# Kernel tuning notes

Hardware: AMD Instinct MI355X
Metric: run time of the kernel (lower is better)

## Reference

```python
import jax, jax.numpy as jnp
import numpy as np

N = 100000
E = 1600000
D_IN = 128
D_OUT = 128

def setup_inputs() -> dict:
    key = jax.random.key(0)
    k1, k2, k3, k4, k5, k6 = jax.random.split(key, 6)
    h = jax.random.normal(k1, (N, D_IN), dtype=jnp.float32)
    # norm ~ deg^{-1/2}; use positive uniform values as stand-in
    norm = jax.random.uniform(k2, (N, 1), dtype=jnp.float32, minval=0.05, maxval=1.0)
    src = jax.random.randint(k3, (E,), 0, N, dtype=jnp.int32)
    dst = jax.random.randint(k4, (E,), 0, N, dtype=jnp.int32)
    weight = jax.random.normal(k5, (D_IN, D_OUT), dtype=jnp.float32) * (2.0 / (D_IN + D_OUT)) ** 0.5
    bias = jnp.zeros((D_OUT,), dtype=jnp.float32)
    return {"h": h, "norm": norm, "src": src, "dst": dst, "weight": weight, "bias": bias}

def reference(h, norm, src, dst, weight, bias):
    n_nodes = h.shape[0]
    hw = h @ weight                      # [N, D_out] dense GEMM
    hw = hw * norm                       # pre-aggregation degree scale
    msgs = hw[src]                       # gather: [E, D_out]
    agg = jax.ops.segment_sum(msgs, dst, num_segments=n_nodes)  # scatter-sum
    out = agg * norm + bias              # post-scale + bias
    return out
```

## Files before the change

### kernel.cpp

```cpp
#include <hip/hip_runtime.h>
#include <hip/hip_bf16.h>

#define D 128
#define D4 32
#define CHUNK 3072
#define MAXB 2048
#define NSEG 8
#define SL 4096

typedef __attribute__((ext_vector_type(8))) short bf16x8;
typedef __attribute__((ext_vector_type(8))) unsigned short ushort8;
typedef __attribute__((ext_vector_type(4))) float f32x4;

static __device__ __forceinline__ unsigned short f2bf(float f) {
    unsigned u = __float_as_uint(f);
    u += 0x7FFFu + ((u >> 16) & 1u);
    return (unsigned short)(u >> 16);
}
static __device__ __forceinline__ float bf2f(unsigned short u) {
    return __uint_as_float(((unsigned)u) << 16);
}

__global__ __launch_bounds__(256) void wcvt_kernel(
    const float* __restrict__ W, unsigned short* __restrict__ Wt)
{
    const int idx = blockIdx.x * 256 + threadIdx.x;
    const float4 w = ((const float4*)W)[idx];
    const int k = idx >> 5;
    const int c = (idx & 31) * 4;
    Wt[(c + 0) * 128 + k] = f2bf(w.x);
    Wt[(c + 1) * 128 + k] = f2bf(w.y);
    Wt[(c + 2) * 128 + k] = f2bf(w.z);
    Wt[(c + 3) * 128 + k] = f2bf(w.w);
}

__global__ __launch_bounds__(512) void gemm_mfma_kernel(
    const float* __restrict__ h, const unsigned short* __restrict__ Wt,
    const float* __restrict__ norm, unsigned short* __restrict__ hwb,
    int n_nodes)
{
    __shared__ unsigned short Bs[128 * 136];

    const int t = threadIdx.x;
    const int row0 = blockIdx.x * 128;

    #pragma unroll
    for (int i = 0; i < 4; ++i) {
        const int idx = t + 512 * i;
        const int c = idx >> 4;
        const int k8 = idx & 15;
        *(ushort8*)&Bs[c * 136 + k8 * 8] = ((const ushort8*)Wt)[idx];
    }
    __syncthreads();

    const int wv = t >> 6;
    const int lane = t & 63;
    const int m = lane & 15;
    const int quad = lane >> 4;

    long gra = row0 + wv * 16 + m;
    if (gra >= n_nodes) gra = n_nodes - 1;
    const float* hrow = h + gra * D;

    f32x4 acc[8];
    #pragma unroll
    for (int nt = 0; nt < 8; ++nt) { f32x4 z = {0.f, 0.f, 0.f, 0.f}; acc[nt] = z; }

    #pragma unroll
    for (int kt = 0; kt < 4; ++kt) {
        const float4 a0 = *(const float4*)(hrow + kt * 32 + quad * 8);
        const float4 a1 = *(const float4*)(hrow + kt * 32 + quad * 8 + 4);
        bf16x8 af;
        unsigned short* ap = (unsigned short*)&af;
        ap[0] = f2bf(a0.x); ap[1] = f2bf(a0.y); ap[2] = f2bf(a0.z); ap[3] = f2bf(a0.w);
        ap[4] = f2bf(a1.x); ap[5] = f2bf(a1.y); ap[6] = f2bf(a1.z); ap[7] = f2bf(a1.w);
        #pragma unroll
        for (int nt = 0; nt < 8; ++nt) {
            const bf16x8 bfr = *(const bf16x8*)&Bs[(nt * 16 + m) * 136 + kt * 32 + quad * 8];
            acc[nt] = __builtin_amdgcn_mfma_f32_16x16x32_bf16(af, bfr, acc[nt], 0, 0, 0);
        }
    }

    float nv[4];
    #pragma unroll
    for (int i = 0; i < 4; ++i) {
        const int gr = row0 + wv * 16 + quad * 4 + i;
        nv[i] = (gr < n_nodes) ? norm[gr] : 0.f;
    }
    #pragma unroll
    for (int nt = 0; nt < 8; ++nt) {
        #pragma unroll
        for (int i = 0; i < 4; ++i) {
            const int gr = row0 + wv * 16 + quad * 4 + i;
            if (gr < n_nodes)
                hwb[(size_t)gr * D + nt * 16 + m] = f2bf(acc[nt][i] * nv[i]);
        }
    }
}

__global__ __launch_bounds__(1024) void hist_kernel(
    const int* __restrict__ dst, int* __restrict__ H,
    unsigned short* __restrict__ hwb, int n_edges, int n_nodes)
{
    __shared__ int lbh[MAXB];
    const int t = threadIdx.x;
    const int g = blockIdx.x;
    for (int i = t; i < MAXB; i += 1024) lbh[i] = 0;
    if (g == 0 && t < 32) {
        ushort4 z; z.x = z.y = z.z = z.w = 0;
        ((ushort4*)(hwb + (size_t)n_nodes * D))[t] = z;
    }
    __syncthreads();
    const int e0 = g * CHUNK;
    const int e1 = min(e0 + CHUNK, n_edges);
    for (int e = e0 + t; e < e1; e += 1024) {
        atomicAdd(&lbh[dst[e] >> 6], 1);
    }
    __syncthreads();
    for (int i = t; i < MAXB; i += 1024) {
        H[(size_t)g * MAXB + i] = lbh[i];
    }
}

__global__ __launch_bounds__(256) void colsum_kernel(
    const int* __restrict__ H, int* __restrict__ PS, int eb)
{
    const int col = blockIdx.x * 256 + threadIdx.x;
    const int seg = blockIdx.y;
    const int glen = (eb + NSEG - 1) / NSEG;
    const int g0 = seg * glen;
    const int g1 = min(g0 + glen, eb);
    int s = 0;
    for (int g = g0; g < g1; ++g) s += H[(size_t)g * MAXB + col];
    PS[seg * MAXB + col] = s;
}

__global__ __launch_bounds__(256) void bucket_scan_kernel(
    const int* __restrict__ PS, int* __restrict__ boff, int* __restrict__ SB)
{
    __shared__ int tmp[256];
    const int t = threadIdx.x;
    int v[8];
    int s = 0;
    #pragma unroll
    for (int k = 0; k < 8; ++k) {
        const int i = t * 8 + k;
        int c = 0;
        #pragma unroll
        for (int sg = 0; sg < NSEG; ++sg) c += PS[sg * MAXB + i];
        v[k] = c; s += c;
    }
    tmp[t] = s;
    __syncthreads();
    for (int ofs = 1; ofs < 256; ofs <<= 1) {
        int x = (t >= ofs) ? tmp[t - ofs] : 0;
        __syncthreads();
        tmp[t] += x;
        __syncthreads();
    }
    int run = tmp[t] - s;
    #pragma unroll
    for (int k = 0; k < 8; ++k) {
        const int i = t * 8 + k;
        boff[i] = run;
        int sb = run;
        #pragma unroll
        for (int sg = 0; sg < NSEG; ++sg) {
            SB[sg * MAXB + i] = sb;
            sb += PS[sg * MAXB + i];
        }
        run += v[k];
    }
    if (t == 255) boff[MAXB] = run;
}

__global__ __launch_bounds__(256) void chunkscan_kernel(
    const int* __restrict__ H, const int* __restrict__ SB,
    int* __restrict__ CO, int eb)
{
    const int b = blockIdx.x * 256 + threadIdx.x;
    const int seg = blockIdx.y;
    const int glen = (eb + NSEG - 1) / NSEG;
    const int g0 = seg * glen;
    const int g1 = min(g0 + glen, eb);
    int run = SB[seg * MAXB + b];
    for (int g = g0; g < g1; ++g) {
        CO[(size_t)g * MAXB + b] = run;
        run += H[(size_t)g * MAXB + b];
    }
}

__global__ __launch_bounds__(1024) void bscatter_kernel(
    const int* __restrict__ src, const int* __restrict__ dst,
    const int* __restrict__ CO,
    unsigned int* __restrict__ ebuf, int n_edges)
{
    __shared__ int lbh[MAXB];
    __shared__ int lofs[MAXB];
    const int t = threadIdx.x;
    const int g = blockIdx.x;
    for (int i = t; i < MAXB; i += 1024) {
        lbh[i] = 0;
        lofs[i] = CO[(size_t)g * MAXB + i];
    }
    __syncthreads();
    const int e0 = g * CHUNK;
    const int e1 = min(e0 + CHUNK, n_edges);
    for (int e = e0 + t; e < e1; e += 1024) {
        const int d = dst[e];
        const int bk = d >> 6;
        const int r = atomicAdd(&lbh[bk], 1);
        ebuf[lofs[bk] + r] = (unsigned)src[e] | ((unsigned)(d & 63) << 17);
    }
}

__global__ __launch_bounds__(256) void fillagg_kernel(
    const unsigned int* __restrict__ ebuf, const int* __restrict__ boff,
    int* __restrict__ srcs_g, const unsigned short* __restrict__ hwb,
    const float* __restrict__ norm, const float* __restrict__ bias,
    float* __restrict__ out, int n_nodes)
{
    __shared__ int slds[SL];
    __shared__ int lcnt[64];
    __shared__ int lcur[64];
    __shared__ int loff[64];
    const int t = threadIdx.x;
    const int b = blockIdx.x;
    const int gn0 = b * 64;

    if (t < 64) lcnt[t] = 0;
    __syncthreads();
    const int w0 = boff[b], w1 = boff[b + 1];
    const int wlen = w1 - w0;
    const bool uselds = (wlen + 480) <= SL;
    const int gbase = w0 + 448 * b;

    for (int e = w0 + t; e < w1; e += 256) {
        atomicAdd(&lcnt[(ebuf[e] >> 17) & 63], 1);
    }
    __syncthreads();
    if (t < 64) {
        const int c = lcnt[t];
        const int p = (c + 7) & ~7;
        int x = p;
        #pragma unroll
        for (int ofs = 1; ofs < 64; ofs <<= 1) {
            const int y = __shfl_up(x, ofs, 64);
            if (t >= ofs) x += y;
        }
        const int base = x - p;
        lcur[t] = base;
        loff[t] = base;
    }
    __syncthreads();
    for (int e = w0 + t; e < w1; e += 256) {
        const unsigned rec = ebuf[e];
        const int loc = (rec >> 17) & 63;
        const int pos = atomicAdd(&lcur[loc], 1);
        const int sv = (int)(rec & 0x1FFFFu);
        if (uselds) slds[pos] = sv; else srcs_g[gbase + pos] = sv;
    }
    for (int w = t; w < 512; w += 256) {
        const int ln = w >> 3, k = w & 7;
        const int gn = gn0 + ln;
        if (gn < n_nodes) {
            const int c = lcnt[ln];
            const int pad = (8 - (c & 7)) & 7;
            if (k < pad) {
                const int pos = loff[ln] + c + k;
                if (uselds) slds[pos] = n_nodes; else srcs_g[gbase + pos] = n_nodes;
            }
        }
    }
    __syncthreads();

    const ushort4* hw4 = (const ushort4*)hwb;
    const int grp = t >> 5;
    const int l = t & 31;
    const float4 bs = ((const float4*)bias)[l];
    for (int nn = 0; nn < 8; ++nn) {
        const int loc = grp * 8 + nn;
        const int gn = gn0 + loc;
        if (gn >= n_nodes) continue;
        const int start = loff[loc];
        const int deg = lcnt[loc];
        const int nb8 = (deg + 7) >> 3;
        float4 acc; acc.x = acc.y = acc.z = acc.w = 0.f;
        int myidx = 0;
        for (int bb = 0; bb < nb8; ++bb) {
            const int q = bb & 3;
            if (q == 0) {
                const int ri = start + bb * 8 + l;
                myidx = uselds ? slds[ri] : srcs_g[gbase + ri];
            }
            ushort4 v[8];
            #pragma unroll
            for (int jj = 0; jj < 8; ++jj) {
                const int s = __shfl(myidx, q * 8 + jj, 32);
                v[jj] = hw4[(long)s * D4 + l];
            }
            #pragma unroll
            for (int jj = 0; jj < 8; ++jj) {
                acc.x += bf2f(v[jj].x);
                acc.y += bf2f(v[jj].y);
                acc.z += bf2f(v[jj].z);
                acc.w += bf2f(v[jj].w);
            }
        }
        const float nv = norm[gn];
        float4 o;
        o.x = acc.x * nv + bs.x;
        o.y = acc.y * nv + bs.y;
        o.z = acc.z * nv + bs.z;
        o.w = acc.w * nv + bs.w;
        ((float4*)out)[(long)gn * D4 + l] = o;
    }
}

__global__ __launch_bounds__(256) void scatter_kernel(
    const unsigned short* __restrict__ hwb, const int* __restrict__ src,
    const int* __restrict__ dst, float* __restrict__ out, int n_edges)
{
    const int idx = blockIdx.x * 256 + threadIdx.x;
    if (idx >= n_edges * D4) return;
    const int e = idx >> 5;
    const int g = idx & 31;
    const int s = src[e];
    const int d = dst[e];
    const ushort4 v = ((const ushort4*)hwb)[(long)s * D4 + g];
    float* o = out + (long)d * D + g * 4;
    atomicAdd(o + 0, bf2f(v.x));
    atomicAdd(o + 1, bf2f(v.y));
    atomicAdd(o + 2, bf2f(v.z));
    atomicAdd(o + 3, bf2f(v.w));
}

__global__ __launch_bounds__(256) void finalize_kernel(
    float* __restrict__ out, const float* __restrict__ norm,
    const float* __restrict__ bias, int n_nodes)
{
    const int idx = blockIdx.x * 256 + threadIdx.x;
    if (idx >= n_nodes * D4) return;
    const int n = idx >> 5;
    const int g = idx & 31;
    float4 v = ((float4*)out)[idx];
    const float nv = norm[n];
    const float4 b = ((const float4*)bias)[g];
    v.x = v.x * nv + b.x;
    v.y = v.y * nv + b.y;
    v.z = v.z * nv + b.z;
    v.w = v.w * nv + b.w;
    ((float4*)out)[idx] = v;
}

extern "C" void kernel_launch(void* const* d_in, const int* in_sizes, int n_in,
                              void* d_out, int out_size, void* d_ws, size_t ws_size,
                              hipStream_t stream) {
    const float* h    = (const float*)d_in[0];
    const float* norm = (const float*)d_in[1];
    const int*   src  = (const int*)d_in[2];
    const int*   dst  = (const int*)d_in[3];
    const float* W    = (const float*)d_in[4];
    const float* bias = (const float*)d_in[5];
    float* out = (float*)d_out;

    const int n_nodes = in_sizes[1];
    const int n_edges = in_sizes[2];

    const int NBUCK = (n_nodes + 63) >> 6;
    const int EB    = (n_edges + CHUNK - 1) / CHUNK;
    const int srcs_len = n_edges + 448 * NBUCK + 64;

    size_t p = 0;
    auto take = [&](size_t bytes) {
        size_t cur = p;
        p += (bytes + 255) & ~(size_t)255;
        return cur;
    };
    const size_t hwb_off  = take(((size_t)n_nodes + 1) * D * sizeof(unsigned short));
    const size_t wt_off   = take((size_t)D * D * sizeof(unsigned short));
    const size_t srcs_off = take((size_t)srcs_len * sizeof(int));
    const size_t ebuf_off = take((size_t)n_edges * sizeof(unsigned int));
    const size_t boff_off = take((MAXB + 1) * sizeof(int));
    const size_t H_off    = take((size_t)EB * MAXB * sizeof(int));
    const size_t PS_off   = take((size_t)NSEG * MAXB * sizeof(int));
    const size_t SB_off   = take((size_t)NSEG * MAXB * sizeof(int));
    const size_t CO_off   = take((size_t)EB * MAXB * sizeof(int));
    const size_t needed = p;

    char* ws = (char*)d_ws;
    unsigned short* hwb = (unsigned short*)(ws + hwb_off);
    unsigned short* Wt  = (unsigned short*)(ws + wt_off);

    wcvt_kernel<<<16, 256, 0, stream>>>(W, Wt);
    gemm_mfma_kernel<<<(n_nodes + 127) / 128, 512, 0, stream>>>(h, Wt, norm, hwb, n_nodes);

    if (ws_size >= needed && NBUCK <= MAXB && n_nodes <= 131072 && EB <= 1024) {
        int* srcs  = (int*)(ws + srcs_off);
        unsigned int* ebuf = (unsigned int*)(ws + ebuf_off);
        int* boff  = (int*)(ws + boff_off);
        int* H     = (int*)(ws + H_off);
        int* PS    = (int*)(ws + PS_off);
        int* SBp   = (int*)(ws + SB_off);
        int* CO    = (int*)(ws + CO_off);

        hist_kernel<<<EB, 1024, 0, stream>>>(dst, H, hwb, n_edges, n_nodes);
        colsum_kernel<<<dim3(MAXB / 256, NSEG), 256, 0, stream>>>(H, PS, EB);
        bucket_scan_kernel<<<1, 256, 0, stream>>>(PS, boff, SBp);
        chunkscan_kernel<<<dim3(MAXB / 256, NSEG), 256, 0, stream>>>(H, SBp, CO, EB);
        bscatter_kernel<<<EB, 1024, 0, stream>>>(src, dst, CO, ebuf, n_edges);
        fillagg_kernel<<<NBUCK, 256, 0, stream>>>(ebuf, boff, srcs, hwb, norm, bias,
                                                  out, n_nodes);
    } else {
        hipMemsetAsync(d_out, 0, (size_t)out_size * sizeof(float), stream);
        const int work = n_edges * D4;
        scatter_kernel<<<(work + 255) / 256, 256, 0, stream>>>(hwb, src, dst, out, n_edges);
        const int work2 = n_nodes * D4;
        finalize_kernel<<<(work2 + 255) / 256, 256, 0, stream>>>(out, norm, bias, n_nodes);
    }
}
```

Measured before the change: 247.1 us.

## Fuse colsum into local chunk scan, stage GEMM output via LDS, double chunk size

Merges the column-sum and chunk-scan passes into one kernel that writes chunk-local offsets plus segment totals, and adds the segment base inside the scatter kernel. This removes one kernel launch and one full pass over the histogram matrix. The GEMM epilogue now stages the bf16 results in shared memory and writes 16-byte vectors per row instead of scattered 2-byte stores. The edge chunk per block is also doubled, which halves the histogram and offset matrix sizes but gives each block more serial work and fewer blocks.

```diff
diff --git a/kernel.cpp b/kernel.cpp
--- a/kernel.cpp
+++ b/kernel.cpp
@@ -3,7 +3,7 @@
 
 #define D 128
 #define D4 32
-#define CHUNK 3072
+#define CHUNK 6144
 #define MAXB 2048
 #define NSEG 8
 #define SL 4096
@@ -87,14 +87,27 @@
         const int gr = row0 + wv * 16 + quad * 4 + i;
         nv[i] = (gr < n_nodes) ? norm[gr] : 0.f;
     }
+
+    __syncthreads();
     #pragma unroll
     for (int nt = 0; nt < 8; ++nt) {
         #pragma unroll
         for (int i = 0; i < 4; ++i) {
-            const int gr = row0 + wv * 16 + quad * 4 + i;
-            if (gr < n_nodes)
-                hwb[(size_t)gr * D + nt * 16 + m] = f2bf(acc[nt][i] * nv[i]);
-        }
+            const int r = wv * 16 + quad * 4 + i;
+            Bs[r * 136 + nt * 16 + m] = f2bf(acc[nt][i] * nv[i]);
+        }
+    }
+    __syncthreads();
+
+    #pragma unroll
+    for (int i2 = 0; i2 < 4; ++i2) {
+        const int idx = t + 512 * i2;
+        const int r = idx >> 4;
+        const int c8 = idx & 15;
+        const int gr = row0 + r;
+        if (gr < n_nodes)
+            *(ushort8*)&hwb[(size_t)gr * D + c8 * 8] =
+                *(const ushort8*)&Bs[r * 136 + c8 * 8];
     }
 }
 
@@ -122,17 +135,21 @@
     }
 }
 
-__global__ __launch_bounds__(256) void colsum_kernel(
-    const int* __restrict__ H, int* __restrict__ PS, int eb)
-{
-    const int col = blockIdx.x * 256 + threadIdx.x;
+__global__ __launch_bounds__(256) void chunkscan_local_kernel(
+    const int* __restrict__ H, int* __restrict__ CO, int* __restrict__ PS,
+    int eb)
+{
+    const int b = blockIdx.x * 256 + threadIdx.x;
     const int seg = blockIdx.y;
     const int glen = (eb + NSEG - 1) / NSEG;
     const int g0 = seg * glen;
     const int g1 = min(g0 + glen, eb);
-    int s = 0;
-    for (int g = g0; g < g1; ++g) s += H[(size_t)g * MAXB + col];
-    PS[seg * MAXB + col] = s;
+    int run = 0;
+    for (int g = g0; g < g1; ++g) {
+        CO[(size_t)g * MAXB + b] = run;
+        run += H[(size_t)g * MAXB + b];
+    }
+    PS[seg * MAXB + b] = run;
 }
 
 __global__ __launch_bounds__(256) void bucket_scan_kernel(
@@ -174,34 +191,20 @@
     if (t == 255) boff[MAXB] = run;
 }
 
-__global__ __launch_bounds__(256) void chunkscan_kernel(
-    const int* __restrict__ H, const int* __restrict__ SB,
-    int* __restrict__ CO, int eb)
-{
-    const int b = blockIdx.x * 256 + threadIdx.x;
-    const int seg = blockIdx.y;
-    const int glen = (eb + NSEG - 1) / NSEG;
-    const int g0 = seg * glen;
-    const int g1 = min(g0 + glen, eb);
-    int run = SB[seg * MAXB + b];
-    for (int g = g0; g < g1; ++g) {
-        CO[(size_t)g * MAXB + b] = run;
-        run += H[(size_t)g * MAXB + b];
-    }
-}
-
 __global__ __launch_bounds__(1024) void bscatter_kernel(
     const int* __restrict__ src, const int* __restrict__ dst,
-    const int* __restrict__ CO,
-    unsigned int* __restrict__ ebuf, int n_edges)
+    const int* __restrict__ CO, const int* __restrict__ SB,
+    unsigned int* __restrict__ ebuf, int n_edges, int eb)
 {
     __shared__ int lbh[MAXB];
     __shared__ int lofs[MAXB];
     const int t = threadIdx.x;
     const int g = blockIdx.x;
+    const int glen = (eb + NSEG - 1) / NSEG;
+    const int seg = g / glen;
     for (int i = t; i < MAXB; i += 1024) {
         lbh[i] = 0;
-        lofs[i] = CO[(size_t)g * MAXB + i];
+        lofs[i] = SB[seg * MAXB + i] + CO[(size_t)g * MAXB + i];
     }
     __syncthreads();
     const int e0 = g * CHUNK;
@@ -405,10 +408,9 @@
         int* CO    = (int*)(ws + CO_off);
 
         hist_kernel<<<EB, 1024, 0, stream>>>(dst, H, hwb, n_edges, n_nodes);
-        colsum_kernel<<<dim3(MAXB / 256, NSEG), 256, 0, stream>>>(H, PS, EB);
+        chunkscan_local_kernel<<<dim3(MAXB / 256, NSEG), 256, 0, stream>>>(H, CO, PS, EB);
         bucket_scan_kernel<<<1, 256, 0, stream>>>(PS, boff, SBp);
-        chunkscan_kernel<<<dim3(MAXB / 256, NSEG), 256, 0, stream>>>(H, SBp, CO, EB);
-        bscatter_kernel<<<EB, 1024, 0, stream>>>(src, dst, CO, ebuf, n_edges);
+        bscatter_kernel<<<EB, 1024, 0, stream>>>(src, dst, CO, SBp, ebuf, n_edges, EB);
         fillagg_kernel<<<NBUCK, 256, 0, stream>>>(ebuf, boff, srcs, hwb, norm, bias,
                                                   out, n_nodes);
     } else {
```

After: 235.4 us. 1.05x faster.
